# Optimization experiments

Measured on AMD Instinct MI355X. Metric: run time of the kernel, lower is better.

Reference implementation:

```python
import jax, jax.numpy as jnp
import numpy as np


def setup_inputs() -> dict:
    key = jax.random.key(0)
    k1, k2 = jax.random.split(key)
    B, C, H, W = 16, 64, 144, 144
    x = jax.random.normal(k1, (B, C, H, W), dtype=jnp.float32)
    y = jax.random.normal(k2, (B, C, H, W), dtype=jnp.float32)
    return {"x": x, "y": y, "shape": 144}


def reference(x, y, shape):
    # Restrict to the [0:shape, 0:shape] spatial window the Python loop covers.
    xs = x[:, :, :shape, :shape]
    ys = y[:, :, :shape, :shape]
    # Per-pixel reductions over batch AND channel (torch .sum() reduces all
    # remaining dims of x[:, :, i, j], i.e. both B and C).
    fz = jnp.einsum('bchw,bchw->hw', xs, ys)        # [shape, shape]
    xx = jnp.einsum('bchw,bchw->hw', xs, xs)
    yy = jnp.einsum('bchw,bchw->hw', ys, ys)
    fm = jnp.sqrt(xx) * jnp.sqrt(yy)
    loss = jnp.sum(jnp.arccos(fz / fm))
    return loss / (shape ** 2)
```

## Files before the change

### kernel.cpp

```cpp
#include <hip/hip_runtime.h>
#include <math.h>


constexpr int PLANE  = 144 * 144;
constexpr int QUADS  = PLANE / 4;
constexpr int BC     = 16 * 64;
constexpr int SPLIT  = 8;
constexpr int BCS    = BC / SPLIT;
constexpr int WAVES  = 8;
constexpr int PPW    = BCS / WAVES;
constexpr int CHUNK  = 8;
constexpr int NCHUNK = PPW / CHUNK;
constexpr int NBLK   = QUADS / 64;
constexpr int B2     = 81;

__global__ __launch_bounds__(512) void spe_partial(const float4* __restrict__ x,
                                                   const float4* __restrict__ y,
                                                   float4* __restrict__ fzp,
                                                   float4* __restrict__ xxp,
                                                   float4* __restrict__ yyp,
                                                   unsigned* __restrict__ counter)
{
    const int tid  = threadIdx.x;
    const int lane = tid & 63;
    const int w    = tid >> 6;
    const int s    = blockIdx.y;
    const int qq   = blockIdx.x * 64 + lane;

    if (blockIdx.x == 0 && blockIdx.y == 0 && tid == 0) *counter = 0u;

    float4 fz = make_float4(0.f, 0.f, 0.f, 0.f);
    float4 xx = make_float4(0.f, 0.f, 0.f, 0.f);
    float4 yy = make_float4(0.f, 0.f, 0.f, 0.f);

    size_t idx = ((size_t)s * BCS + w) * QUADS + (size_t)qq;
    const size_t pstep = (size_t)WAVES * QUADS;

    #pragma unroll 1
    for (int c = 0; c < NCHUNK; ++c) {
        float4 a[CHUNK], b[CHUNK];
        size_t i0 = idx;
        #pragma unroll
        for (int u = 0; u < CHUNK; ++u) {
            a[u] = x[i0];
            b[u] = y[i0];
            i0 += pstep;
        }
        __builtin_amdgcn_sched_barrier(0);
        #pragma unroll
        for (int u = 0; u < CHUNK; ++u) {
            fz.x = fmaf(a[u].x, b[u].x, fz.x); fz.y = fmaf(a[u].y, b[u].y, fz.y);
            fz.z = fmaf(a[u].z, b[u].z, fz.z); fz.w = fmaf(a[u].w, b[u].w, fz.w);
            xx.x = fmaf(a[u].x, a[u].x, xx.x); xx.y = fmaf(a[u].y, a[u].y, xx.y);
            xx.z = fmaf(a[u].z, a[u].z, xx.z); xx.w = fmaf(a[u].w, a[u].w, xx.w);
            yy.x = fmaf(b[u].x, b[u].x, yy.x); yy.y = fmaf(b[u].y, b[u].y, yy.y);
            yy.z = fmaf(b[u].z, b[u].z, yy.z); yy.w = fmaf(b[u].w, b[u].w, yy.w);
        }
        idx += pstep * CHUNK;
    }

    __shared__ float4 lf[WAVES][64], lx[WAVES][64], ly[WAVES][64];
    lf[w][lane] = fz; lx[w][lane] = xx; ly[w][lane] = yy;
    __syncthreads();

    if (tid < 64) {
        float4 F = lf[0][tid], X = lx[0][tid], Y = ly[0][tid];
        #pragma unroll
        for (int wv = 1; wv < WAVES; ++wv) {
            F.x += lf[wv][tid].x; F.y += lf[wv][tid].y;
            F.z += lf[wv][tid].z; F.w += lf[wv][tid].w;
            X.x += lx[wv][tid].x; X.y += lx[wv][tid].y;
            X.z += lx[wv][tid].z; X.w += lx[wv][tid].w;
            Y.x += ly[wv][tid].x; Y.y += ly[wv][tid].y;
            Y.z += ly[wv][tid].z; Y.w += ly[wv][tid].w;
        }
        const size_t o = (size_t)s * QUADS + (size_t)(blockIdx.x * 64 + tid);
        fzp[o] = F; xxp[o] = X; yyp[o] = Y;
    }
}

__global__ __launch_bounds__(256) void spe_stage2(const float* __restrict__ fzp,
                                                  const float* __restrict__ xxp,
                                                  const float* __restrict__ yyp,
                                                  float* __restrict__ bsum,
                                                  unsigned* __restrict__ counter,
                                                  float* __restrict__ out)
{
    const int t = threadIdx.x;
    const int p = blockIdx.x * 256 + t;

    float F = 0.f, X = 0.f, Y = 0.f;
    #pragma unroll
    for (int s = 0; s < SPLIT; ++s) {
        F += fzp[s * PLANE + p];
        X += xxp[s * PLANE + p];
        Y += yyp[s * PLANE + p];
    }
    float r = F / (sqrtf(X) * sqrtf(Y));
    r = fminf(1.f, fmaxf(-1.f, r));
    float v = acosf(r);

    __shared__ float l[4];
    __shared__ int lastFlag;
    #pragma unroll
    for (int off = 32; off >= 1; off >>= 1) v += __shfl_down(v, off);
    if ((t & 63) == 0) l[t >> 6] = v;
    __syncthreads();

    if (t == 0) {
        bsum[blockIdx.x] = l[0] + l[1] + l[2] + l[3];
        __threadfence();
        unsigned old = atomicAdd(counter, 1u);
        lastFlag = (old == B2 - 1);
    }
    __syncthreads();

    if (lastFlag && t == 0) {
        __threadfence();
        float tot = 0.f;
        for (int i = 0; i < B2; ++i) tot += bsum[i];
        out[0] = tot * (1.0f / (float)PLANE);
    }
}

extern "C" void kernel_launch(void* const* d_in, const int* in_sizes, int n_in,
                              void* d_out, int out_size, void* d_ws, size_t ws_size,
                              hipStream_t stream) {
    const float4* x = (const float4*)d_in[0];
    const float4* y = (const float4*)d_in[1];

    float* ws   = (float*)d_ws;
    float* fzp  = ws;
    float* xxp  = ws + (size_t)SPLIT * PLANE;
    float* yyp  = ws + (size_t)2 * SPLIT * PLANE;
    float* bsum = ws + (size_t)3 * SPLIT * PLANE;
    unsigned* counter = (unsigned*)(bsum + B2);
    float* out  = (float*)d_out;

    dim3 grid(NBLK, SPLIT);
    spe_partial<<<grid, 512, 0, stream>>>(x, y, (float4*)fzp, (float4*)xxp,
                                          (float4*)yyp, counter);
    spe_stage2<<<B2, 256, 0, stream>>>(fzp, xxp, yyp, bsum, counter, out);
}
```

Baseline: 36.38 us.

## Double-buffer partial-reduction loads with inline-asm global loads and manual waitcnt

Replaces the chunked load-then-compute loop in the partial reduction kernel with a two-stage software pipeline. Each stage holds two x/y float4 pairs, and the next stage's loads are issued while the current stage is being accumulated. Explicit s_waitcnt vmcnt controls the waits instead of draining all loads per chunk. Loads now use inline-asm global_load_dwordx4 with an SGPR base and a 32-bit VGPR byte offset, which cuts 64-bit address arithmetic. In exchange, fewer loads are in flight per wave than with the previous 8-deep chunk, and correctness depends on the hand-placed waitcnts.

```diff
diff --git a/kernel.cpp b/kernel.cpp
--- a/kernel.cpp
+++ b/kernel.cpp
@@ -9,13 +9,31 @@
 constexpr int BCS    = BC / SPLIT;
 constexpr int WAVES  = 8;
 constexpr int PPW    = BCS / WAVES;
-constexpr int CHUNK  = 8;
-constexpr int NCHUNK = PPW / CHUNK;
 constexpr int NBLK   = QUADS / 64;
 constexpr int B2     = 81;
+constexpr unsigned PSTRIDE = (unsigned)(WAVES * QUADS * 16);
 
-__global__ __launch_bounds__(512) void spe_partial(const float4* __restrict__ x,
-                                                   const float4* __restrict__ y,
+__device__ __forceinline__ float4 gload(const float* __restrict__ base, unsigned off) {
+    float4 r;
+    asm volatile("global_load_dwordx4 %0, %1, %2"
+                 : "=v"(r)
+                 : "v"(off), "s"(base)
+                 : "memory");
+    return r;
+}
+
+__device__ __forceinline__ void fmac3(const float4& a, const float4& b,
+                                      float4& fz, float4& xx, float4& yy) {
+    fz.x = fmaf(a.x, b.x, fz.x); fz.y = fmaf(a.y, b.y, fz.y);
+    fz.z = fmaf(a.z, b.z, fz.z); fz.w = fmaf(a.w, b.w, fz.w);
+    xx.x = fmaf(a.x, a.x, xx.x); xx.y = fmaf(a.y, a.y, xx.y);
+    xx.z = fmaf(a.z, a.z, xx.z); xx.w = fmaf(a.w, a.w, xx.w);
+    yy.x = fmaf(b.x, b.x, yy.x); yy.y = fmaf(b.y, b.y, yy.y);
+    yy.z = fmaf(b.z, b.z, yy.z); yy.w = fmaf(b.w, b.w, yy.w);
+}
+
+__global__ __launch_bounds__(512) void spe_partial(const float* __restrict__ xf,
+                                                   const float* __restrict__ yf,
                                                    float4* __restrict__ fzp,
                                                    float4* __restrict__ xxp,
                                                    float4* __restrict__ yyp,
@@ -33,30 +51,34 @@
     float4 xx = make_float4(0.f, 0.f, 0.f, 0.f);
     float4 yy = make_float4(0.f, 0.f, 0.f, 0.f);
 
-    size_t idx = ((size_t)s * BCS + w) * QUADS + (size_t)qq;
-    const size_t pstep = (size_t)WAVES * QUADS;
+    unsigned off = (((unsigned)s * BCS + (unsigned)w) * QUADS + (unsigned)qq) * 16u;
 
-    #pragma unroll 1
-    for (int c = 0; c < NCHUNK; ++c) {
-        float4 a[CHUNK], b[CHUNK];
-        size_t i0 = idx;
+    float4 bx[2][2], by[2][2];
+    #pragma unroll
+    for (int k = 0; k < 2; ++k) {
         #pragma unroll
-        for (int u = 0; u < CHUNK; ++u) {
-            a[u] = x[i0];
-            b[u] = y[i0];
-            i0 += pstep;
+        for (int u = 0; u < 2; ++u) {
+            bx[k][u] = gload(xf, off);
+            by[k][u] = gload(yf, off);
+            off += PSTRIDE;
         }
+    }
+    #pragma unroll
+    for (int c = 0; c < 8; ++c) {
+        if (c < 7) asm volatile("s_waitcnt vmcnt(4)" ::: "memory");
+        else       asm volatile("s_waitcnt vmcnt(0)" ::: "memory");
         __builtin_amdgcn_sched_barrier(0);
+        const int cur = c & 1;
         #pragma unroll
-        for (int u = 0; u < CHUNK; ++u) {
-            fz.x = fmaf(a[u].x, b[u].x, fz.x); fz.y = fmaf(a[u].y, b[u].y, fz.y);
-            fz.z = fmaf(a[u].z, b[u].z, fz.z); fz.w = fmaf(a[u].w, b[u].w, fz.w);
-            xx.x = fmaf(a[u].x, a[u].x, xx.x); xx.y = fmaf(a[u].y, a[u].y, xx.y);
-            xx.z = fmaf(a[u].z, a[u].z, xx.z); xx.w = fmaf(a[u].w, a[u].w, xx.w);
-            yy.x = fmaf(b[u].x, b[u].x, yy.x); yy.y = fmaf(b[u].y, b[u].y, yy.y);
-            yy.z = fmaf(b[u].z, b[u].z, yy.z); yy.w = fmaf(b[u].w, b[u].w, yy.w);
+        for (int u = 0; u < 2; ++u) fmac3(bx[cur][u], by[cur][u], fz, xx, yy);
+        if (c < 6) {
+            #pragma unroll
+            for (int u = 0; u < 2; ++u) {
+                bx[cur][u] = gload(xf, off);
+                by[cur][u] = gload(yf, off);
+                off += PSTRIDE;
+            }
         }
-        idx += pstep * CHUNK;
     }
 
     __shared__ float4 lf[WAVES][64], lx[WAVES][64], ly[WAVES][64];
@@ -126,8 +148,8 @@
 extern "C" void kernel_launch(void* const* d_in, const int* in_sizes, int n_in,
                               void* d_out, int out_size, void* d_ws, size_t ws_size,
                               hipStream_t stream) {
-    const float4* x = (const float4*)d_in[0];
-    const float4* y = (const float4*)d_in[1];
+    const float* x = (const float*)d_in[0];
+    const float* y = (const float*)d_in[1];
 
     float* ws   = (float*)d_ws;
     float* fzp  = ws;
```

Result: no change. 35.98 us (-1.1%).
